# Kernel optimization log

Hardware: AMD Instinct MI355X
Metric: run time of the kernel (lower is better)

Reference implementation:

```python
import jax, jax.numpy as jnp
import numpy as np

DECAY = 0.6
GAIN = 0.4
LN_EPS = 1e-5


def ema_scan(x, axis):
    # s_t = DECAY*s_{t-1} + GAIN*x_t, s_{-1}=0, along `axis`; vectorized over all other dims
    xm = jnp.moveaxis(x, axis, 0)
    def step(s, xt):
        s = DECAY * s + GAIN * xt
        return s, s
    _, ys = jax.lax.scan(step, jnp.zeros_like(xm[0]), xm)
    return jnp.moveaxis(ys, 0, axis)


def setup_inputs() -> dict:
    key = jax.random.key(0)
    ks = jax.random.split(key, 8)
    B, H, W, D = 8, 96, 96, 192
    C = 2 * D  # inner_dim
    s_in = 1.0 / np.sqrt(D)
    s_out = 1.0 / np.sqrt(C)
    return {
        "x": jax.random.normal(ks[0], (B, H, W, D), dtype=jnp.float32),
        "W_in": jax.random.uniform(ks[1], (D, C), minval=-s_in, maxval=s_in, dtype=jnp.float32),
        "b_in": jax.random.uniform(ks[2], (C,), minval=-s_in, maxval=s_in, dtype=jnp.float32),
        "conv_w": jax.random.uniform(ks[3], (C, 1, 3, 3), minval=-1.0/3.0, maxval=1.0/3.0, dtype=jnp.float32),
        "ln_g": jnp.ones((C,), dtype=jnp.float32),
        "ln_b": jnp.zeros((C,), dtype=jnp.float32),
        "W_out": jax.random.uniform(ks[4], (C, D), minval=-s_out, maxval=s_out, dtype=jnp.float32),
        "b_out": jax.random.uniform(ks[5], (D,), minval=-s_out, maxval=s_out, dtype=jnp.float32),
    }


def reference(x, W_in, b_in, conv_w, ln_g, ln_b, W_out, b_out):
    C = W_in.shape[1]
    # in_proj: [B,H,W,D] -> [B,H,W,C]
    proj = jnp.einsum("bhwd,dc->bhwc", x, W_in) + b_in
    # channels-first for depthwise conv: [B,C,H,W]
    cf = jnp.transpose(proj, (0, 3, 1, 2))
    local = jax.lax.conv_general_dilated(
        cf, conv_w, window_strides=(1, 1), padding="SAME",
        feature_group_count=C,
        dimension_numbers=("NCHW", "OIHW", "NCHW"))
    # four directional EMA scans
    lr = ema_scan(local, 3)
    rl = jnp.flip(ema_scan(jnp.flip(local, 3), 3), 3)
    tb = ema_scan(local, 2)
    bt = jnp.flip(ema_scan(jnp.flip(local, 2), 2), 2)
    mixed = 0.25 * (lr + rl + tb + bt) + local
    # back to channels-last, layernorm over C
    mixed = jnp.transpose(mixed, (0, 2, 3, 1))
    mu = jnp.mean(mixed, axis=-1, keepdims=True)
    var = jnp.mean(jnp.square(mixed - mu), axis=-1, keepdims=True)
    normed = (mixed - mu) * jax.lax.rsqrt(var + LN_EPS) * ln_g + ln_b
    return jnp.einsum("bhwc,cd->bhwd", normed, W_out) + b_out
```

## Files before the change

### kernel.cpp

```cpp
#include <hip/hip_runtime.h>
#include <hip/hip_bf16.h>

#define NB 8
#define NH 96
#define NW 96
#define ND 192
#define NC 384
#define NPOS (NB*NH*NW)
#define NELEM ((size_t)NPOS*NC)

#define DECAY 0.6f
#define GAIN 0.4f
#define D16 2.8211099e-4f

typedef __attribute__((ext_vector_type(8))) short bf16x8;
typedef __attribute__((ext_vector_type(4))) float f32x4;
typedef __attribute__((ext_vector_type(4))) unsigned short us4;

__device__ inline unsigned short f2bf(float f) {
  unsigned u = __float_as_uint(f);
  u += 0x7fff + ((u >> 16) & 1);
  return (unsigned short)(u >> 16);
}
__device__ inline float bf2f(unsigned short u) {
  return __uint_as_float((unsigned)u << 16);
}

__device__ inline void gload16(const void* g, void* l) {
  __builtin_amdgcn_global_load_lds(
      (const __attribute__((address_space(1))) void*)g,
      (__attribute__((address_space(3))) void*)l, 16, 0, 0);
}

__device__ inline f32x4 ldf4(const float* p) {
  return *reinterpret_cast<const f32x4*>(p);
}
__device__ inline f32x4 ldb4(const unsigned short* p) {
  us4 v = *reinterpret_cast<const us4*>(p);
  return (f32x4){bf2f(v.x), bf2f(v.y), bf2f(v.z), bf2f(v.w)};
}
__device__ inline void stb4(unsigned short* p, f32x4 v) {
  us4 o = {f2bf(v[0]), f2bf(v[1]), f2bf(v[2]), f2bf(v[3])};
  *reinterpret_cast<us4*>(p) = o;
}
__device__ inline uint2 pk4(f32x4 v) {
  us4 o = {f2bf(v[0]), f2bf(v[1]), f2bf(v[2]), f2bf(v[3])};
  uint2 r; __builtin_memcpy(&r, &o, 8); return r;
}
__device__ inline f32x4 up4(uint2 p) {
  return (f32x4){__uint_as_float(p.x << 16), __uint_as_float(p.x & 0xffff0000u),
                 __uint_as_float(p.y << 16), __uint_as_float(p.y & 0xffff0000u)};
}
__device__ inline bf16x8 pk8(f32x4 a, f32x4 b) {
  bf16x8 r;
#pragma unroll
  for (int i = 0; i < 4; ++i) {
    r[i]     = (short)f2bf(a[i]);
    r[i + 4] = (short)f2bf(b[i]);
  }
  return r;
}
__device__ inline unsigned mswz(int row, int byteInRow) {
  return (unsigned)(row * 768 + (byteInRow ^ ((row & 7) << 4)));
}

__global__ __launch_bounds__(256) void cvt_w_kernel(
    const float* __restrict__ Wi, const float* __restrict__ Wo,
    unsigned short* __restrict__ WtI, unsigned short* __restrict__ WtO) {
  int idx = blockIdx.x * 256 + threadIdx.x;
  if (idx < ND * NC) {
    int k = idx / NC, c = idx % NC;
    WtI[c * ND + k] = f2bf(Wi[idx]);
  } else {
    int j = idx - ND * NC;
    int k = j / ND, d = j % ND;
    WtO[d * NC + k] = f2bf(Wo[j]);
  }
}

template<int K, int N, int BN>
__global__ __launch_bounds__(256) void gemm_kernel(
    const float* __restrict__ A32,
    const unsigned short* __restrict__ Bt,
    const float* __restrict__ bias,
    unsigned short* __restrict__ C) {
  constexpr int NF = BN / 32;
  __shared__ __align__(16) unsigned short lsA[8192];
  __shared__ __align__(16) unsigned short lsB[4 * BN * 8];

  const int tid = threadIdx.x;
  const int lane = tid & 63;
  const int wid = tid >> 6;
  const int wm = wid >> 1, wn = wid & 1;
  const int kg = lane >> 4, r16 = lane & 15;
  const int m0 = blockIdx.x * 128;
  const int n0 = blockIdx.y * BN;

  const float* srcAf[4]; float* dstAf[4];
  {
    float* lsAf = (float*)lsA;
#pragma unroll
    for (int p = 0; p < 4; ++p) {
      int s = tid + p * 256;
      int row = s >> 3, g = s & 7;
      int gg = g ^ (row & 7);
      srcAf[p] = A32 + (size_t)(m0 + row) * K + gg * 4;
      dstAf[p] = lsAf + s * 4;
    }
  }
  const unsigned short* srcB0 = Bt + (size_t)(n0 + (tid & (BN - 1))) * K + (tid / BN) * 8;
  const int sb1 = tid + 256;
  const unsigned short* srcBh = Bt + (size_t)(n0 + (sb1 & 127)) * K + (sb1 >> 7) * 8;

  int boff[NF];
#pragma unroll
  for (int n = 0; n < NF; ++n)
    boff[n] = (kg * BN + wn * (BN / 2) + n * 16 + r16) * 8;

  f32x4 acc[4][NF];
  float bv[NF];
#pragma unroll
  for (int n = 0; n < NF; ++n) bv[n] = bias[n0 + wn * (BN / 2) + n * 16 + r16];
#pragma unroll
  for (int m = 0; m < 4; ++m)
#pragma unroll
    for (int n = 0; n < NF; ++n)
      acc[m][n] = (f32x4){bv[n], bv[n], bv[n], bv[n]};

  for (int ks = 0; ks < K / 32; ++ks) {
    const int ke = ks * 32;
#pragma unroll
    for (int p = 0; p < 4; ++p) gload16(srcAf[p] + ke, dstAf[p]);
    gload16(srcB0 + ke, &lsB[tid * 8]);
    if constexpr (BN == 128) gload16(srcBh + ke, &lsB[(tid + 256) * 8]);
    __syncthreads();
    bf16x8 af[4], bfr[NF];
    {
      const float* lsAf = (const float*)lsA;
      const int r7 = r16 & 7;
#pragma unroll
      for (int m = 0; m < 4; ++m) {
        const int rowf = wm * 64 + m * 16 + r16;
        const float* rp = lsAf + rowf * 32;
        f32x4 a0 = *reinterpret_cast<const f32x4*>(rp + ((2 * kg) ^ r7) * 4);
        f32x4 a1 = *reinterpret_cast<const f32x4*>(rp + ((2 * kg + 1) ^ r7) * 4);
        af[m] = pk8(a0, a1);
      }
    }
#pragma unroll
    for (int n = 0; n < NF; ++n)
      bfr[n] = *reinterpret_cast<const bf16x8*>(&lsB[boff[n]]);
#pragma unroll
    for (int m = 0; m < 4; ++m)
#pragma unroll
      for (int n = 0; n < NF; ++n)
        acc[m][n] = __builtin_amdgcn_mfma_f32_16x16x32_bf16(af[m], bfr[n], acc[m][n], 0, 0, 0);
    __syncthreads();
  }

#pragma unroll
  for (int m = 0; m < 4; ++m) {
    const int row = m0 + wm * 64 + m * 16 + kg * 4;
#pragma unroll
    for (int n = 0; n < NF; ++n) {
      const int col = n0 + wn * (BN / 2) + n * 16 + r16;
#pragma unroll
      for (int j = 0; j < 4; ++j)
        C[(size_t)(row + j) * N + col] = f2bf(acc[m][n][j]);
    }
  }
}

__global__ __launch_bounds__(576) void dh_kernel(
    const unsigned short* __restrict__ proj, const float* __restrict__ cw,
    unsigned short* __restrict__ loc_t, unsigned short* __restrict__ acc_t) {
  __shared__ f32x4 agf[6][96];
  __shared__ f32x4 agb[6][96];
  const int tid = threadIdx.x;
  const int c4 = tid % 96;
  const int seg = tid / 96;
  const int w0 = seg * 16;
  const int bid = blockIdx.x;
  const int bh = (bid & 7) * NH + (bid >> 3);
  const int h = bh % NH;
  const int b = bh / NH;

  f32x4 raw[9];
  const float* cwp = cw + (size_t)c4 * 36;
#pragma unroll
  for (int i = 0; i < 9; ++i) raw[i] = ldf4(cwp + i * 4);
  f32x4 qq[9];
#pragma unroll
  for (int tap = 0; tap < 9; ++tap)
#pragma unroll
    for (int c = 0; c < 4; ++c)
      qq[tap][c] = raw[(c * 9 + tap) >> 2][(c * 9 + tap) & 3];

  const bool hm = (h > 0), hp = (h < NH - 1);
  const unsigned short* rowm = proj + ((size_t)(bh - 1) * NW) * NC + c4 * 4;
  const unsigned short* rowc = proj + ((size_t)bh * NW) * NC + c4 * 4;
  const unsigned short* rowp = proj + ((size_t)(bh + 1) * NW) * NC + c4 * 4;
  unsigned short* tbase = loc_t + ((size_t)(b * NW + w0) * NH + h) * NC + c4 * 4;
  unsigned short* abase = acc_t + ((size_t)(b * NW + w0) * NH + h) * NC + c4 * 4;
  const size_t wst = (size_t)NH * NC;

  const f32x4 z = {0.f, 0.f, 0.f, 0.f};
  f32x4 colL[3], colC[3], colR[3];
  if (w0 > 0) {
    colL[0] = hm ? ldb4(rowm + (size_t)(w0 - 1) * NC) : z;
    colL[1] = ldb4(rowc + (size_t)(w0 - 1) * NC);
    colL[2] = hp ? ldb4(rowp + (size_t)(w0 - 1) * NC) : z;
  } else { colL[0] = z; colL[1] = z; colL[2] = z; }
  colC[0] = hm ? ldb4(rowm + (size_t)w0 * NC) : z;
  colC[1] = ldb4(rowc + (size_t)w0 * NC);
  colC[2] = hp ? ldb4(rowp + (size_t)w0 * NC) : z;

  uint2 xr[16];
#pragma unroll
  for (int i = 0; i < 16; ++i) {
    const int w = w0 + i;
    if (w + 1 < NW) {
      colR[0] = hm ? ldb4(rowm + (size_t)(w + 1) * NC) : z;
      colR[1] = ldb4(rowc + (size_t)(w + 1) * NC);
      colR[2] = hp ? ldb4(rowp + (size_t)(w + 1) * NC) : z;
    } else { colR[0] = z; colR[1] = z; colR[2] = z; }
    f32x4 a = colL[0] * qq[0] + colC[0] * qq[1] + colR[0] * qq[2]
            + colL[1] * qq[3] + colC[1] * qq[4] + colR[1] * qq[5]
            + colL[2] * qq[6] + colC[2] * qq[7] + colR[2] * qq[8];
    xr[i] = pk4(a);
    *reinterpret_cast<uint2*>(tbase + (size_t)i * wst) = xr[i];
    colL[0] = colC[0]; colL[1] = colC[1]; colL[2] = colC[2];
    colC[0] = colR[0]; colC[1] = colR[1]; colC[2] = colR[2];
  }

  f32x4 Af = z, Ab = z;
#pragma unroll
  for (int i = 0; i < 16; ++i) Af = DECAY * Af + GAIN * up4(xr[i]);
#pragma unroll
  for (int i = 15; i >= 0; --i) Ab = DECAY * Ab + GAIN * up4(xr[i]);
  agf[seg][c4] = Af; agb[seg][c4] = Ab;
  __syncthreads();
  f32x4 Fin = z, Bin = z;
  if (seg >= 1) Fin = agf[seg - 1][c4];
  if (seg >= 2) Fin += D16 * agf[seg - 2][c4];
  if (seg <= 4) Bin = agb[seg + 1][c4];
  if (seg <= 3) Bin += D16 * agb[seg + 2][c4];

  uint2 bwp[16];
  f32x4 Bs = Bin;
#pragma unroll
  for (int i = 15; i >= 0; --i) {
    Bs = DECAY * Bs + GAIN * up4(xr[i]);
    bwp[i] = pk4(Bs);
  }
  f32x4 Fs = Fin;
#pragma unroll
  for (int i = 0; i < 16; ++i) {
    Fs = DECAY * Fs + GAIN * up4(xr[i]);
    stb4(abase + (size_t)i * wst, Fs + up4(bwp[i]));
  }
}

__global__ __launch_bounds__(576) void vgemm_kernel(
    const unsigned short* __restrict__ loc_t, const unsigned short* __restrict__ acc_t,
    const float* __restrict__ g, const float* __restrict__ bb,
    const unsigned short* __restrict__ WtO, const float* __restrict__ bo,
    float* __restrict__ out) {
  __shared__ __align__(16) unsigned short mix[96 * NC];
  __shared__ __align__(16) unsigned short lsB[2][6144];
  f32x4* ag = (f32x4*)mix;
  char* mixc = (char*)mix;
  const int tid = threadIdx.x;
  const int lane = tid & 63;
  const int kg = lane >> 4, r16 = lane & 15;
  const int c4 = tid % 96;
  const int seg = tid / 96;
  const int h0 = seg * 16;
  const int bw = blockIdx.x;

  {
    int s = tid, kgg = s / 192, d = s % 192;
    gload16(WtO + (size_t)d * NC + kgg * 8, &lsB[0][s * 8]);
    if (tid < 192) {
      int s2 = tid + 576, kg2 = s2 / 192, d2 = s2 % 192;
      gload16(WtO + (size_t)d2 * NC + kg2 * 8, &lsB[0][s2 * 8]);
    }
  }

  const size_t base = ((size_t)bw * NH + h0) * NC + c4 * 4;
  const unsigned short* lp = loc_t + base;
  const unsigned short* ap = acc_t + base;
  uint2 xr[16], avp[16];
#pragma unroll
  for (int i = 0; i < 16; ++i) xr[i] = *reinterpret_cast<const uint2*>(lp + (size_t)i * NC);
#pragma unroll
  for (int i = 0; i < 16; ++i) avp[i] = *reinterpret_cast<const uint2*>(ap + (size_t)i * NC);

  const f32x4 z = {0.f, 0.f, 0.f, 0.f};
  f32x4 Af = z, Ab = z;
#pragma unroll
  for (int i = 0; i < 16; ++i) Af = DECAY * Af + GAIN * up4(xr[i]);
#pragma unroll
  for (int i = 15; i >= 0; --i) Ab = DECAY * Ab + GAIN * up4(xr[i]);
  ag[seg * 96 + c4] = Af;
  ag[576 + seg * 96 + c4] = Ab;
  __syncthreads();
  f32x4 Fin = z, Bin = z;
  if (seg >= 1) Fin = ag[(seg - 1) * 96 + c4];
  if (seg >= 2) Fin += D16 * ag[(seg - 2) * 96 + c4];
  if (seg <= 4) Bin = ag[576 + (seg + 1) * 96 + c4];
  if (seg <= 3) Bin += D16 * ag[576 + (seg + 2) * 96 + c4];
  __syncthreads();

  f32x4 Bs = Bin;
#pragma unroll
  for (int i = 15; i >= 0; --i) {
    f32x4 xv = up4(xr[i]);
    Bs = DECAY * Bs + GAIN * xv;
    f32x4 part = xv + 0.25f * (up4(avp[i]) + Bs);
    stb4((unsigned short*)(mixc + mswz(h0 + i, c4 * 8)), part);
  }
  f32x4 Fs = Fin;
#pragma unroll
  for (int i = 0; i < 16; ++i) {
    Fs = DECAY * Fs + GAIN * up4(xr[i]);
    unsigned short* slot = (unsigned short*)(mixc + mswz(h0 + i, c4 * 8));
    stb4(slot, ldb4(slot) + 0.25f * Fs);
  }
  __syncthreads();

  const int wave = tid >> 6;
  const int cb = lane * 6;
  {
    float gv[6], bv6[6];
#pragma unroll
    for (int i = 0; i < 6; ++i) { gv[i] = g[cb + i]; bv6[i] = bb[cb + i]; }
    for (int h = wave; h < NH; h += 9) {
      ushort2* p0 = (ushort2*)(mixc + mswz(h, lane * 12));
      ushort2* p1 = (ushort2*)(mixc + mswz(h, lane * 12 + 4));
      ushort2* p2 = (ushort2*)(mixc + mswz(h, lane * 12 + 8));
      ushort2 a2 = *p0, b2 = *p1, c2 = *p2;
      float v[6];
      v[0] = bf2f(a2.x); v[1] = bf2f(a2.y);
      v[2] = bf2f(b2.x); v[3] = bf2f(b2.y);
      v[4] = bf2f(c2.x); v[5] = bf2f(c2.y);
      float sm = 0.f, s2 = 0.f;
#pragma unroll
      for (int i = 0; i < 6; ++i) { sm += v[i]; s2 += v[i] * v[i]; }
#pragma unroll
      for (int o = 32; o > 0; o >>= 1) {
        sm += __shfl_xor(sm, o, 64);
        s2 += __shfl_xor(s2, o, 64);
      }
      float mu = sm * (1.f / NC);
      float r = rsqrtf(s2 * (1.f / NC) - mu * mu + 1e-5f);
      unsigned short o6[6];
#pragma unroll
      for (int i = 0; i < 6; ++i)
        o6[i] = f2bf((v[i] - mu) * r * gv[i] + bv6[i]);
      *p0 = (ushort2){o6[0], o6[1]};
      *p1 = (ushort2){o6[2], o6[3]};
      *p2 = (ushort2){o6[4], o6[5]};
    }
  }
  __syncthreads();

  const int wm = wave / 3, wn = wave % 3;
  f32x4 acc[2][4];
  {
    float bv[4];
#pragma unroll
    for (int n = 0; n < 4; ++n) bv[n] = bo[wn * 64 + n * 16 + r16];
#pragma unroll
    for (int m = 0; m < 2; ++m)
#pragma unroll
      for (int n = 0; n < 4; ++n)
        acc[m][n] = (f32x4){bv[n], bv[n], bv[n], bv[n]};
  }
  for (int ks = 0; ks < 12; ++ks) {
    if (ks < 11) {
      int s = tid, kgg = s / 192, d = s % 192;
      gload16(WtO + (size_t)d * NC + (ks + 1) * 32 + kgg * 8, &lsB[(ks + 1) & 1][s * 8]);
      if (tid < 192) {
        int s2 = tid + 576, kg2 = s2 / 192, d2 = s2 % 192;
        gload16(WtO + (size_t)d2 * NC + (ks + 1) * 32 + kg2 * 8, &lsB[(ks + 1) & 1][s2 * 8]);
      }
    }
    const unsigned short* bufp = lsB[ks & 1];
    bf16x8 af[2], bfr[4];
#pragma unroll
    for (int m = 0; m < 2; ++m) {
      const int row = wm * 32 + m * 16 + r16;
      af[m] = *reinterpret_cast<const bf16x8*>(mixc + mswz(row, ks * 64 + kg * 16));
    }
#pragma unroll
    for (int n = 0; n < 4; ++n)
      bfr[n] = *reinterpret_cast<const bf16x8*>(&bufp[(kg * 192 + wn * 64 + n * 16 + r16) * 8]);
#pragma unroll
    for (int m = 0; m < 2; ++m)
#pragma unroll
      for (int n = 0; n < 4; ++n)
        acc[m][n] = __builtin_amdgcn_mfma_f32_16x16x32_bf16(af[m], bfr[n], acc[m][n], 0, 0, 0);
    __syncthreads();
  }

  const int bq = bw / NW, wq = bw % NW;
#pragma unroll
  for (int m = 0; m < 2; ++m) {
    const int hbase = wm * 32 + m * 16 + kg * 4;
#pragma unroll
    for (int n = 0; n < 4; ++n) {
      const int d = wn * 64 + n * 16 + r16;
#pragma unroll
      for (int j = 0; j < 4; ++j)
        out[((size_t)(bq * NH + hbase + j) * NW + wq) * ND + d] = acc[m][n][j];
    }
  }
}

extern "C" void kernel_launch(void* const* d_in, const int* in_sizes, int n_in,
                              void* d_out, int out_size, void* d_ws, size_t ws_size,
                              hipStream_t stream) {
  const float* x    = (const float*)d_in[0];
  const float* W_in = (const float*)d_in[1];
  const float* b_in = (const float*)d_in[2];
  const float* cw   = (const float*)d_in[3];
  const float* ln_g = (const float*)d_in[4];
  const float* ln_b = (const float*)d_in[5];
  const float* W_out= (const float*)d_in[6];
  const float* b_out= (const float*)d_in[7];
  float* out = (float*)d_out;

  unsigned short* wsu   = (unsigned short*)d_ws;
  unsigned short* proj  = wsu;
  unsigned short* loc_t = proj + 28311552;
  unsigned short* acc_t = loc_t + 28311552;
  unsigned short* WtI   = acc_t + 28311552;
  unsigned short* WtO   = WtI + 73728;

  cvt_w_kernel<<<(2 * ND * NC) / 256, 256, 0, stream>>>(W_in, W_out, WtI, WtO);
  {
    dim3 g(NPOS / 128, NC / 128);
    gemm_kernel<ND, NC, 128><<<g, 256, 0, stream>>>(x, WtI, b_in, proj);
  }
  dh_kernel<<<NB * NH, 576, 0, stream>>>(proj, cw, loc_t, acc_t);
  vgemm_kernel<<<NB * NW, 576, 0, stream>>>(loc_t, acc_t, ln_g, ln_b,
                                            WtO, b_out, out);
}
```

Measured before the change: 190.9 us.

## Split vertical-scan GEMM kernel into two half-column blocks with halo carry-in

Each (b,w) column is now handled by two blocks of 48 rows instead of one block of 96. Each block recomputes the EMA carry from the 16 rows just outside its half (with D8/D16 decay factors) instead of sharing it through shared memory. This halves LDS use per block so more blocks can be resident, and doubles the grid from 768 to 1536 blocks. In exchange it re-reads a 16-row halo of loc_t, reloads the full W_out slice in every block, and gives each wave half the MFMA work.

```diff
diff --git a/kernel.cpp b/kernel.cpp
--- a/kernel.cpp
+++ b/kernel.cpp
@@ -11,6 +11,7 @@
 
 #define DECAY 0.6f
 #define GAIN 0.4f
+#define D8  1.679616e-2f
 #define D16 2.8211099e-4f
 
 typedef __attribute__((ext_vector_type(8))) short bf16x8;
@@ -266,17 +267,20 @@
     const float* __restrict__ g, const float* __restrict__ bb,
     const unsigned short* __restrict__ WtO, const float* __restrict__ bo,
     float* __restrict__ out) {
-  __shared__ __align__(16) unsigned short mix[96 * NC];
+  __shared__ __align__(16) unsigned short mix[48 * NC];
   __shared__ __align__(16) unsigned short lsB[2][6144];
-  f32x4* ag = (f32x4*)mix;
+  f32x4* AFs = (f32x4*)mix;
+  f32x4* ABs = AFs + 8 * 96;
   char* mixc = (char*)mix;
   const int tid = threadIdx.x;
   const int lane = tid & 63;
   const int kg = lane >> 4, r16 = lane & 15;
   const int c4 = tid % 96;
   const int seg = tid / 96;
-  const int h0 = seg * 16;
-  const int bw = blockIdx.x;
+  const int bx = blockIdx.x;
+  const int half = bx & 1;
+  const int bw = bx >> 1;
+  const int H0 = half * 48;
 
   {
     int s = tid, kgg = s / 192, d = s % 192;
@@ -287,44 +291,71 @@
     }
   }
 
-  const size_t base = ((size_t)bw * NH + h0) * NC + c4 * 4;
-  const unsigned short* lp = loc_t + base;
-  const unsigned short* ap = acc_t + base;
-  uint2 xr[16], avp[16];
-#pragma unroll
-  for (int i = 0; i < 16; ++i) xr[i] = *reinterpret_cast<const uint2*>(lp + (size_t)i * NC);
-#pragma unroll
-  for (int i = 0; i < 16; ++i) avp[i] = *reinterpret_cast<const uint2*>(ap + (size_t)i * NC);
+  const size_t cbase = ((size_t)bw * NH + H0 + seg * 8) * NC + c4 * 4;
+  const unsigned short* lp = loc_t + cbase;
+  uint2 xr[8];
+#pragma unroll
+  for (int i = 0; i < 8; ++i)
+    xr[i] = *reinterpret_cast<const uint2*>(lp + (size_t)i * NC);
 
   const f32x4 z = {0.f, 0.f, 0.f, 0.f};
+  uint2 wr[8];
+  if (tid < 192) {
+    const int hw = (half == 1) ? (32 + seg * 8) : (48 + seg * 8);
+    const unsigned short* wp = loc_t + ((size_t)bw * NH + hw) * NC + c4 * 4;
+#pragma unroll
+    for (int i = 0; i < 8; ++i)
+      wr[i] = *reinterpret_cast<const uint2*>(wp + (size_t)i * NC);
+  }
+
   f32x4 Af = z, Ab = z;
 #pragma unroll
-  for (int i = 0; i < 16; ++i) Af = DECAY * Af + GAIN * up4(xr[i]);
-#pragma unroll
-  for (int i = 15; i >= 0; --i) Ab = DECAY * Ab + GAIN * up4(xr[i]);
-  ag[seg * 96 + c4] = Af;
-  ag[576 + seg * 96 + c4] = Ab;
+  for (int i = 0; i < 8; ++i) Af = DECAY * Af + GAIN * up4(xr[i]);
+#pragma unroll
+  for (int i = 7; i >= 0; --i) Ab = DECAY * Ab + GAIN * up4(xr[i]);
+  AFs[(2 + seg) * 96 + c4] = Af;
+  ABs[seg * 96 + c4] = Ab;
+  if (tid < 192) {
+    f32x4 wa = z;
+    if (half == 1) {
+#pragma unroll
+      for (int i = 0; i < 8; ++i) wa = DECAY * wa + GAIN * up4(wr[i]);
+      AFs[seg * 96 + c4] = wa;
+      ABs[(6 + seg) * 96 + c4] = z;
+    } else {
+#pragma unroll
+      for (int i = 7; i >= 0; --i) wa = DECAY * wa + GAIN * up4(wr[i]);
+      ABs[(6 + seg) * 96 + c4] = wa;
+      AFs[seg * 96 + c4] = z;
+    }
+  }
+
+  const unsigned short* ap = acc_t + cbase;
+  uint2 avp[8];
+#pragma unroll
+  for (int i = 0; i < 8; ++i)
+    avp[i] = *reinterpret_cast<const uint2*>(ap + (size_t)i * NC);
+
   __syncthreads();
-  f32x4 Fin = z, Bin = z;
-  if (seg >= 1) Fin = ag[(seg - 1) * 96 + c4];
-  if (seg >= 2) Fin += D16 * ag[(seg - 2) * 96 + c4];
-  if (seg <= 4) Bin = ag[576 + (seg + 1) * 96 + c4];
-  if (seg <= 3) Bin += D16 * ag[576 + (seg + 2) * 96 + c4];
+  f32x4 Fin = AFs[(seg + 1) * 96 + c4] + D8 * AFs[seg * 96 + c4];
+  if (seg >= 1) Fin += D16 * AFs[(seg - 1) * 96 + c4];
+  f32x4 Bin = ABs[(seg + 1) * 96 + c4] + D8 * ABs[(seg + 2) * 96 + c4];
+  if (seg <= 4) Bin += D16 * ABs[(seg + 3) * 96 + c4];
   __syncthreads();
 
   f32x4 Bs = Bin;
 #pragma unroll
-  for (int i = 15; i >= 0; --i) {
+  for (int i = 7; i >= 0; --i) {
     f32x4 xv = up4(xr[i]);
     Bs = DECAY * Bs + GAIN * xv;
     f32x4 part = xv + 0.25f * (up4(avp[i]) + Bs);
-    stb4((unsigned short*)(mixc + mswz(h0 + i, c4 * 8)), part);
+    stb4((unsigned short*)(mixc + mswz(seg * 8 + i, c4 * 8)), part);
   }
   f32x4 Fs = Fin;
 #pragma unroll
-  for (int i = 0; i < 16; ++i) {
+  for (int i = 0; i < 8; ++i) {
     Fs = DECAY * Fs + GAIN * up4(xr[i]);
-    unsigned short* slot = (unsigned short*)(mixc + mswz(h0 + i, c4 * 8));
+    unsigned short* slot = (unsigned short*)(mixc + mswz(seg * 8 + i, c4 * 8));
     stb4(slot, ldb4(slot) + 0.25f * Fs);
   }
   __syncthreads();
@@ -335,7 +366,7 @@
     float gv[6], bv6[6];
 #pragma unroll
     for (int i = 0; i < 6; ++i) { gv[i] = g[cb + i]; bv6[i] = bb[cb + i]; }
-    for (int h = wave; h < NH; h += 9) {
+    for (int h = wave; h < 48; h += 9) {
       ushort2* p0 = (ushort2*)(mixc + mswz(h, lane * 12));
       ushort2* p1 = (ushort2*)(mixc + mswz(h, lane * 12 + 4));
       ushort2* p2 = (ushort2*)(mixc + mswz(h, lane * 12 + 8));
@@ -366,16 +397,14 @@
   __syncthreads();
 
   const int wm = wave / 3, wn = wave % 3;
-  f32x4 acc[2][4];
+  f32x4 acc[4];
   {
     float bv[4];
 #pragma unroll
     for (int n = 0; n < 4; ++n) bv[n] = bo[wn * 64 + n * 16 + r16];
 #pragma unroll
-    for (int m = 0; m < 2; ++m)
-#pragma unroll
-      for (int n = 0; n < 4; ++n)
-        acc[m][n] = (f32x4){bv[n], bv[n], bv[n], bv[n]};
+    for (int n = 0; n < 4; ++n)
+      acc[n] = (f32x4){bv[n], bv[n], bv[n], bv[n]};
   }
   for (int ks = 0; ks < 12; ++ks) {
     if (ks < 11) {
@@ -387,34 +416,25 @@
       }
     }
     const unsigned short* bufp = lsB[ks & 1];
-    bf16x8 af[2], bfr[4];
-#pragma unroll
-    for (int m = 0; m < 2; ++m) {
-      const int row = wm * 32 + m * 16 + r16;
-      af[m] = *reinterpret_cast<const bf16x8*>(mixc + mswz(row, ks * 64 + kg * 16));
-    }
+    bf16x8 af, bfr[4];
+    af = *reinterpret_cast<const bf16x8*>(mixc + mswz(wm * 16 + r16, ks * 64 + kg * 16));
 #pragma unroll
     for (int n = 0; n < 4; ++n)
       bfr[n] = *reinterpret_cast<const bf16x8*>(&bufp[(kg * 192 + wn * 64 + n * 16 + r16) * 8]);
 #pragma unroll
-    for (int m = 0; m < 2; ++m)
-#pragma unroll
-      for (int n = 0; n < 4; ++n)
-        acc[m][n] = __builtin_amdgcn_mfma_f32_16x16x32_bf16(af[m], bfr[n], acc[m][n], 0, 0, 0);
+    for (int n = 0; n < 4; ++n)
+      acc[n] = __builtin_amdgcn_mfma_f32_16x16x32_bf16(af, bfr[n], acc[n], 0, 0, 0);
     __syncthreads();
   }
 
   const int bq = bw / NW, wq = bw % NW;
-#pragma unroll
-  for (int m = 0; m < 2; ++m) {
-    const int hbase = wm * 32 + m * 16 + kg * 4;
-#pragma unroll
-    for (int n = 0; n < 4; ++n) {
-      const int d = wn * 64 + n * 16 + r16;
-#pragma unroll
-      for (int j = 0; j < 4; ++j)
-        out[((size_t)(bq * NH + hbase + j) * NW + wq) * ND + d] = acc[m][n][j];
-    }
+  const int hbase = H0 + wm * 16 + kg * 4;
+#pragma unroll
+  for (int n = 0; n < 4; ++n) {
+    const int d = wn * 64 + n * 16 + r16;
+#pragma unroll
+    for (int j = 0; j < 4; ++j)
+      out[((size_t)(bq * NH + hbase + j) * NW + wq) * ND + d] = acc[n][j];
   }
 }
 
@@ -444,6 +464,6 @@
     gemm_kernel<ND, NC, 128><<<g, 256, 0, stream>>>(x, WtI, b_in, proj);
   }
   dh_kernel<<<NB * NH, 576, 0, stream>>>(proj, cw, loc_t, acc_t);
-  vgemm_kernel<<<NB * NW, 576, 0, stream>>>(loc_t, acc_t, ln_g, ln_b,
-                                            WtO, b_out, out);
-}
+  vgemm_kernel<<<NB * NW * 2, 576, 0, stream>>>(loc_t, acc_t, ln_g, ln_b,
+                                                WtO, b_out, out);
+}
```

After: 203.2 us. 6.5% more time.
